# Performance work log

Hardware: AMD Instinct MI355X
Metric: run time of the kernel (lower is better)

Reference implementation:

```python
import jax, jax.numpy as jnp
import numpy as np
from jax import lax

H = 16          # heads
K1, K2 = 3, 3   # kernel_size
LN_EPS = 1e-5


def _ln(x, g, b):
    m = jnp.mean(x, axis=-1, keepdims=True)
    v = jnp.mean(jnp.square(x - m), axis=-1, keepdims=True)
    return (x - m) * lax.rsqrt(v + LN_EPS) * g + b


def _gelu(x):
    return jax.nn.gelu(x, approximate=False)  # torch nn.GELU default (erf)


def setup_inputs() -> dict:
    key = jax.random.key(0)
    B, T, D, Th = 4, 1024, 1024, 256
    C = 2 * D  # context_dim
    ks = jax.random.split(key, 16)

    def w(k, shape):
        fan_in = shape[0]
        return (jax.random.normal(k, shape, jnp.float32) / np.sqrt(fan_in)).astype(jnp.float32)

    inp = {
        'x': jax.random.normal(ks[0], (B, T, D), jnp.float32),
        'historical_data': jax.random.normal(ks[1], (B, Th, D), jnp.float32),
        'Wq': w(ks[2], (D, D)),
        'Wk': w(ks[3], (D, D)),
        'Wv': w(ks[4], (D, D)),
        'hist_W': w(ks[5], (D, C)), 'hist_b': jnp.zeros((C,), jnp.float32),
        'hist_ln_g': jnp.ones((C,), jnp.float32), 'hist_ln_b': jnp.zeros((C,), jnp.float32),
        'ctx_W1': w(ks[6], (C, C // 4)), 'ctx_b1': jnp.zeros((C // 4,), jnp.float32),
        'ctx_W2': w(ks[7], (C // 4, 1)), 'ctx_b2': jnp.zeros((1,), jnp.float32),
        'kg_W1': w(ks[8], (C, D)), 'kg_b1': jnp.zeros((D,), jnp.float32),
        'kg_ln_g': jnp.ones((D,), jnp.float32), 'kg_ln_b': jnp.zeros((D,), jnp.float32),
        'kg_W2': w(ks[9], (D, H * K1 * K2)), 'kg_b2': jnp.zeros((H * K1 * K2,), jnp.float32),
        'proj_W': w(ks[10], (D, D)), 'proj_b': jnp.zeros((D,), jnp.float32),
        'causal_mask': jnp.triu(jnp.ones((T, T), bool), k=1),  # True = masked
    }
    return inp


def reference(x, historical_data, Wq, Wk, Wv, hist_W, hist_b, hist_ln_g, hist_ln_b,
              ctx_W1, ctx_b1, ctx_W2, ctx_b2, kg_W1, kg_b1, kg_ln_g, kg_ln_b,
              kg_W2, kg_b2, proj_W, proj_b, causal_mask):
    B, T, D = x.shape
    hd = D // H
    scale = hd ** -0.5

    # qkv projections (no bias), split heads -> [B, H, T, hd]
    q = (x @ Wq).reshape(B, T, H, hd).transpose(0, 2, 1, 3)
    k = (x @ Wk).reshape(B, T, H, hd).transpose(0, 2, 1, 3)
    v = (x @ Wv).reshape(B, T, H, hd).transpose(0, 2, 1, 3)

    attn = jnp.einsum('bhqd,bhkd->bhqk', q, k) * scale  # [B,H,T,T]

    # --- causal context from history ---
    eh = _gelu(_ln(historical_data @ hist_W + hist_b, hist_ln_g, hist_ln_b))  # [B,Th,C]
    aw = _gelu(eh @ ctx_W1 + ctx_b1) @ ctx_W2 + ctx_b2                        # [B,Th,1]
    aw = jax.nn.softmax(aw, axis=1)
    cc = jnp.sum(eh * aw, axis=1)                                             # [B,C]

    # --- per-(batch,head) 3x3 kernels ---
    kp = _gelu(_ln(cc @ kg_W1 + kg_b1, kg_ln_g, kg_ln_b)) @ kg_W2 + kg_b2     # [B,H*9]
    kernels = jax.nn.softmax(kp.reshape(B, H, K1 * K2), axis=-1)
    kernels = kernels.reshape(B * H, 1, K1, K2)

    # zero masked scores, then mix neighbors via grouped conv2d (cross-correlation)
    mask = causal_mask[None, None]  # [1,1,T,T]
    attn0 = jnp.where(mask, 0.0, attn).reshape(1, B * H, T, T)
    attn = lax.conv_general_dilated(
        attn0, kernels, window_strides=(1, 1),
        padding=((K1 // 2, K1 // 2), (K2 // 2, K2 // 2)),
        feature_group_count=B * H,
        dimension_numbers=('NCHW', 'OIHW', 'NCHW'),
    ).reshape(B, H, T, T)

    attn = jnp.where(mask, -jnp.inf, attn)
    p = jax.nn.softmax(attn, axis=-1)
    out = jnp.einsum('bhqk,bhkd->bhqd', p, v)           # [B,H,T,hd]
    out = out.transpose(0, 2, 1, 3).reshape(B, T, D)
    return out @ proj_W + proj_b
```

## Files before the change

kernel.cpp:

```cpp
#include <hip/hip_runtime.h>
#include <hip/hip_bf16.h>
#include <math.h>

#define DEV static __device__ __forceinline__

typedef __attribute__((ext_vector_type(4))) float f32x4;
typedef __attribute__((ext_vector_type(8))) __bf16 bf16x8;
typedef __attribute__((ext_vector_type(8))) short s16x8;
typedef __attribute__((ext_vector_type(2))) _Float16 h16x2;

DEV float b2f(short v){ unsigned u = ((unsigned)(unsigned short)v) << 16; float f; __builtin_memcpy(&f, &u, 4); return f; }
DEV short f2b(float f){ unsigned u; __builtin_memcpy(&u, &f, 4); unsigned r = (u + 0x7fffu + ((u >> 16) & 1u)) >> 16; return (short)r; }
DEV short f2h(float f){ _Float16 h = (_Float16)f; short s; __builtin_memcpy(&s, &h, 2); return s; }
DEV h16x2 u2h2(unsigned u){ h16x2 h; __builtin_memcpy(&h, &u, 4); return h; }
DEV float gelu_f(float v){ return 0.5f * v * (1.0f + erff(v * 0.70710678118654752f)); }

DEV void gload16(const void* g, void* l) {
  __builtin_amdgcn_global_load_lds((const __attribute__((address_space(1))) unsigned int*)g,
                                   (__attribute__((address_space(3))) unsigned int*)l, 16, 0, 0);
}

DEV void xy_swz(int& bx, int& by, int nx, int ny) {
  int lin = by * nx + bx;
  int q = (nx * ny) >> 3;
  int l2 = (lin & 7) * q + (lin >> 3);
  bx = l2 % nx; by = l2 / nx;
}

__global__ __launch_bounds__(256) void k_cast_all(const float* __restrict__ x, const float* __restrict__ hist,
                                                  short* __restrict__ xb, short* __restrict__ histb){
  int bid = blockIdx.x;
  const float* in; short* out; int i;
  if (bid < 2048) { in = x; out = xb; i = (bid * 256 + threadIdx.x) * 8; }
  else            { in = hist; out = histb; i = ((bid - 2048) * 256 + threadIdx.x) * 8; }
  f32x4 a = *(const f32x4*)&in[i];
  f32x4 b = *(const f32x4*)&in[i + 4];
  s16x8 o;
  o[0]=f2b(a[0]); o[1]=f2b(a[1]); o[2]=f2b(a[2]); o[3]=f2b(a[3]);
  o[4]=f2b(b[0]); o[5]=f2b(b[1]); o[6]=f2b(b[2]); o[7]=f2b(b[3]);
  *(s16x8*)&out[i] = o;
}

__global__ __launch_bounds__(256) void k_zero_qk_pads(short* __restrict__ q, short* __restrict__ kk){
  int idx = blockIdx.x * 256 + threadIdx.x;
  int bh = idx >> 5, c = idx & 31;
  int which = c >> 3, chunk = c & 7;
  short* base = (which < 2) ? q : kk;
  size_t off = (size_t)bh * 1026 * 64 + ((which & 1) ? (size_t)1025 * 64 : 0) + chunk * 8;
  s16x8 zz = {};
  *(s16x8*)&base[off] = zz;
}

DEV void tcast_tile(const float* __restrict__ W, short* __restrict__ Wt, int K, int N, int tx, int ty){
  __shared__ float tile[32][33];
  int nb = tx * 32, kb = ty * 32;
  int tid = threadIdx.x;
  int c = tid & 31, r0 = tid >> 5;
  #pragma unroll
  for (int r = r0; r < 32; r += 8) tile[r][c] = W[(size_t)(kb + r) * N + nb + c];
  __syncthreads();
  #pragma unroll
  for (int r = r0; r < 32; r += 8) Wt[(size_t)(nb + r) * K + kb + c] = f2b(tile[c][r]);
}
__global__ __launch_bounds__(256) void k_tcast_all(const float* __restrict__ Wq, const float* __restrict__ Wk,
                                                   const float* __restrict__ Wv, const float* __restrict__ projW,
                                                   const float* __restrict__ histW, const float* __restrict__ ctxW1,
                                                   short* __restrict__ wqkvt, short* __restrict__ wptb,
                                                   short* __restrict__ whtb, short* __restrict__ wc1tb){
  int bid = blockIdx.x;
  const float* W; short* Wt; int K, N, tx, ty;
  if (bid < 4096) {
    int seg = bid >> 10, t = bid & 1023;
    tx = t & 31; ty = t >> 5; K = 1024; N = 1024;
    if      (seg == 0) { W = Wq;    Wt = wqkvt; }
    else if (seg == 1) { W = Wk;    Wt = wqkvt + 1024*1024; }
    else if (seg == 2) { W = Wv;    Wt = wqkvt + 2*1024*1024; }
    else               { W = projW; Wt = wptb; }
  } else if (bid < 6144) {
    int t = bid - 4096; tx = t & 63; ty = t >> 6; K = 1024; N = 2048; W = histW; Wt = whtb;
  } else {
    int t = bid - 6144; tx = t & 15; ty = t >> 4; K = 2048; N = 512; W = ctxW1; Wt = wc1tb;
  }
  tcast_tile(W, Wt, K, N, tx, ty);
}

DEV void gemm_core(const short* __restrict__ A, const short* __restrict__ Bt,
                   int K, int lda, int ldb, int m0, int n0,
                   short* lA, short* lB, f32x4 acc[4][4])
{
  const int tid = threadIdx.x;
  const int lane = tid & 63;
  const int w = tid >> 6;
  const int wr = (w >> 1) * 64, wc = (w & 1) * 64;
  const int lr = lane & 15, lk = (lane >> 4) * 8;
  for (int kt = 0; kt < K; kt += 64) {
    __syncthreads();
    #pragma unroll
    for (int i = 0; i < 4; ++i) {
      int off = i * 2048 + tid * 8;
      int r = off >> 6, c = off & 63;
      gload16(&A[(size_t)(m0 + r) * lda + kt + c], &lA[off]);
      gload16(&Bt[(size_t)(n0 + r) * ldb + kt + c], &lB[off]);
    }
    __syncthreads();
    #pragma unroll
    for (int kk = 0; kk < 64; kk += 32) {
      bf16x8 af[4], bfr[4];
      #pragma unroll
      for (int mi = 0; mi < 4; ++mi) af[mi] = *(bf16x8*)&lA[(wr + mi*16 + lr)*64 + kk + lk];
      #pragma unroll
      for (int ni = 0; ni < 4; ++ni) bfr[ni] = *(bf16x8*)&lB[(wc + ni*16 + lr)*64 + kk + lk];
      #pragma unroll
      for (int mi = 0; mi < 4; ++mi)
        #pragma unroll
        for (int ni = 0; ni < 4; ++ni)
          acc[mi][ni] = __builtin_amdgcn_mfma_f32_16x16x32_bf16(af[mi], bfr[ni], acc[mi][ni], 0, 0, 0);
    }
  }
}

__global__ __launch_bounds__(256) void k_gemm_f32out(const short* __restrict__ A, const short* __restrict__ Bt,
                                                     float* __restrict__ Cout, const float* __restrict__ bias,
                                                     int N, int K, int doGelu)
{
  __shared__ __align__(16) short lds[2 * 128 * 64];
  f32x4 acc[4][4] = {};
  int bx = blockIdx.x, by = blockIdx.y;
  xy_swz(bx, by, gridDim.x, gridDim.y);
  int m0 = by * 128, n0 = bx * 128;
  gemm_core(A, Bt, K, K, K, m0, n0, lds, lds + 128*64, acc);
  int lane = threadIdx.x & 63, w = threadIdx.x >> 6;
  int wr = (w>>1)*64, wc = (w&1)*64, lr4 = (lane>>4)*4, lc = lane & 15;
  #pragma unroll
  for (int mi = 0; mi < 4; ++mi)
    #pragma unroll
    for (int ni = 0; ni < 4; ++ni)
      #pragma unroll
      for (int r = 0; r < 4; ++r) {
        int row = m0 + wr + mi*16 + lr4 + r;
        int col = n0 + wc + ni*16 + lc;
        float v = acc[mi][ni][r] + bias[col];
        if (doGelu) v = gelu_f(v);
        Cout[(size_t)row * N + col] = v;
      }
}

__global__ __launch_bounds__(256) void k_gemm_qkv(const short* __restrict__ xb, const short* __restrict__ wqkvt,
                                                  short* __restrict__ q, short* __restrict__ kk, short* __restrict__ vt)
{
  __shared__ __align__(16) short lds[128 * 136];
  f32x4 acc[4][4] = {};
  int bx = blockIdx.x, by = blockIdx.y;
  xy_swz(bx, by, gridDim.x, gridDim.y);
  int m0 = by * 128, n0 = bx * 128;
  gemm_core(xb, wqkvt, 1024, 1024, 1024, m0, n0, lds, lds + 128*64, acc);
  int tid = threadIdx.x, lane = tid & 63, w = tid >> 6;
  int wr = (w>>1)*64, wc = (w&1)*64, lr4 = (lane>>4)*4, lc = lane & 15;
  int bb = m0 >> 10, tm0 = m0 & 1023;
  int s = n0 >> 10, dn0 = n0 & 1023;
  __syncthreads();
  if (s < 2) {
    short* dst = (s == 0) ? q : kk;
    #pragma unroll
    for (int mi = 0; mi < 4; ++mi)
      #pragma unroll
      for (int ni = 0; ni < 4; ++ni)
        #pragma unroll
        for (int r = 0; r < 4; ++r)
          lds[(wr + mi*16 + lr4 + r) * 136 + wc + ni*16 + lc] = f2b(acc[mi][ni][r]);
    __syncthreads();
    #pragma unroll
    for (int it = 0; it < 8; ++it) {
      int idx = it * 256 + tid;
      int row = idx >> 4, ch = (idx & 15) * 8;
      int dfull = dn0 + ch;
      *(s16x8*)&dst[((size_t)(bb*16 + (dfull >> 6)) * 1026 + 1 + tm0 + row) * 64 + (dfull & 63)]
          = *(s16x8*)&lds[row * 136 + ch];
    }
  } else {
    #pragma unroll
    for (int mi = 0; mi < 4; ++mi)
      #pragma unroll
      for (int ni = 0; ni < 4; ++ni)
        #pragma unroll
        for (int r = 0; r < 4; ++r)
          lds[(wc + ni*16 + lc) * 136 + wr + mi*16 + lr4 + r] = f2b(acc[mi][ni][r]);
    __syncthreads();
    #pragma unroll
    for (int it = 0; it < 8; ++it) {
      int idx = it * 256 + tid;
      int nl = idx >> 4, mc = (idx & 15) * 8;
      int dfull = dn0 + nl;
      *(s16x8*)&vt[(((size_t)(bb*16 + (dfull >> 6)) * 64 + (dfull & 63)) << 10) + tm0 + mc]
          = *(s16x8*)&lds[nl * 136 + mc];
    }
  }
}

constexpr int ASTR = 152;

DEV void conv_chunk(const short* sS, int g, int c,
                    const h16x2 wp01[3], const h16x2 wp2z[3], float o[8]) {
  #pragma unroll
  for (int dr = 0; dr < 3; ++dr) {
    int base = (g + dr) * ASTR + 8 + c;
    const unsigned* W = (const unsigned*)&sS[base];
    unsigned U0 = W[0], U1 = W[1], U2 = W[2], U3 = W[3];
    unsigned hm1 = (unsigned short)sS[base - 1];
    unsigned hp8 = (unsigned short)sS[base + 8];
    unsigned P0 = hm1 | (U0 << 16);
    unsigned P2 = (U0 >> 16) | (U1 << 16);
    unsigned P4 = (U1 >> 16) | (U2 << 16);
    unsigned P6 = (U2 >> 16) | (U3 << 16);
    unsigned P8 = (U3 >> 16) | (hp8 << 16);
    unsigned P9 = hp8;
    unsigned pr[10] = {P0, U0, P2, U1, P4, U2, P6, U3, P8, P9};
    h16x2 a = wp01[dr], bz = wp2z[dr];
    #pragma unroll
    for (int t = 0; t < 8; ++t) {
      o[t] = __builtin_amdgcn_fdot2(a,  u2h2(pr[t]),     o[t], false);
      o[t] = __builtin_amdgcn_fdot2(bz, u2h2(pr[t + 2]), o[t], false);
    }
  }
}

__global__ __launch_bounds__(512, 4) void k_attn(const short* __restrict__ q, const short* __restrict__ kkg,
                                                 const short* __restrict__ vt, const float* __restrict__ kern,
                                                 short* __restrict__ O)
{
  __shared__ __align__(16) short lQ[130 * 64];
  __shared__ __align__(16) short lK[144 * 64];
  __shared__ __align__(16) short lS[130 * ASTR];
  __shared__ float sInv[128];

  int bh = blockIdx.y, b = bh >> 4, h = bh & 15;
  int qt = (bh >= 32) ? 7 - blockIdx.x : blockIdx.x;
  int m0 = qt * 128;
  int tid = threadIdx.x;
  int w = tid >> 6, lane = tid & 63;
  int lr = lane & 15, lk = (lane >> 4) * 8;

  const short* qp = q   + (size_t)bh * 1026 * 64;
  const short* kp = kkg + (size_t)bh * 1026 * 64;

  h16x2 wp01[3], wp2z[3];
  #pragma unroll
  for (int a = 0; a < 3; ++a) {
    wp01[a][0] = (_Float16)kern[bh * 9 + a * 3 + 0];
    wp01[a][1] = (_Float16)kern[bh * 9 + a * 3 + 1];
    wp2z[a][0] = (_Float16)kern[bh * 9 + a * 3 + 2];
    wp2z[a][1] = (_Float16)0.0f;
  }

  s16x8 zz = {};
  for (int t = tid; t < 130 * 8; t += 512)
    gload16(&qp[((size_t)(m0 + (t >> 3))) * 64 + (t & 7) * 8], &lQ[t * 8]);

  f32x4 pacc[4] = {};
  float psum = 0.0f;
  int g = tid >> 2, qc = tid & 3;

  for (int ct = 0; ct <= qt; ++ct) {
    int n0 = ct * 128;
    for (int t = tid; t < 130 * 8; t += 512)
      gload16(&kp[((size_t)(n0 + (t >> 3))) * 64 + (t & 7) * 8], &lK[t * 8]);
    for (int t = tid; t < 14 * 8; t += 512)
      *(s16x8*)&lK[(130 * 8 + t) * 8] = zz;
    __syncthreads();

    int ntmax = (ct == qt) ? (w + 2) : 9;
    for (int nt = 0; nt < ntmax; ++nt) {
      f32x4 acc = {};
      #pragma unroll
      for (int kk = 0; kk < 64; kk += 32) {
        bf16x8 aq = *(bf16x8*)&lQ[(1 + w * 16 + lr) * 64 + kk + lk];
        bf16x8 bk = *(bf16x8*)&lK[(nt * 16 + lr) * 64 + kk + lk];
        acc = __builtin_amdgcn_mfma_f32_16x16x32_bf16(aq, bk, acc, 0, 0, 0);
      }
      int cloc = nt * 16 + lr - 1;
      if (cloc <= 128) {
        #pragma unroll
        for (int r = 0; r < 4; ++r) {
          int rl = w * 16 + (lane >> 4) * 4 + r;
          float v = acc[r] * 0.125f;
          if (n0 + cloc > m0 + rl) v = 0.0f;
          lS[(rl + 1) * ASTR + 8 + cloc] = f2h(v);
        }
      }
    }
    {
      int hr = -1, hl = 0;
      if (tid < 130) { hr = 0; hl = tid; }
      else if (tid >= 256 && tid < 386) { hr = 129; hl = tid - 256; }
      if (hr >= 0) {
        int cloc = hl - 1;
        int gq = m0 - 1 + hr;
        int gk = n0 + cloc;
        float s = 0.0f;
        if (gq >= 0 && gq < 1024 && gk >= 0 && gk <= gq) {
          #pragma unroll
          for (int kk2 = 0; kk2 < 64; kk2 += 8) {
            s16x8 qv = *(s16x8*)&lQ[hr * 64 + kk2];
            s16x8 kv = *(s16x8*)&lK[(cloc + 1) * 64 + kk2];
            #pragma unroll
            for (int j = 0; j < 8; ++j) s += b2f(qv[j]) * b2f(kv[j]);
          }
          s *= 0.125f;
        }
        lS[hr * ASTR + 8 + cloc] = f2h(s);
      }
    }
    __syncthreads();

    s16x8 ps[4];
    #pragma unroll
    for (int j = 0; j < 4; ++j) {
      int c = qc * 32 + j * 8;
      bool live = (ct < qt) || (c <= g);
      float o[8] = {};
      if (live) conv_chunk(lS, g, c, wp01, wp2z, o);
      int glim = (ct == qt) ? g : 127;
      s16x8 po;
      #pragma unroll
      for (int t = 0; t < 8; ++t) {
        float e = (live && (c + t <= glim)) ? __expf(o[t]) : 0.0f;
        psum += e;
        po[t] = f2b(e);
      }
      ps[j] = po;
    }
    __syncthreads();

    #pragma unroll
    for (int j = 0; j < 4; ++j)
      *(s16x8*)&lS[g * ASTR + 8 + qc * 32 + j * 8] = ps[j];
    __syncthreads();

    int kl = 128;
    if (ct == qt) { kl = ((w * 16 + 16 + 31) >> 5) << 5; if (kl > 128) kl = 128; }
    for (int k0 = 0; k0 < kl; k0 += 32) {
      bf16x8 a = *(bf16x8*)&lS[(w * 16 + lr) * ASTR + 8 + k0 + lk];
      #pragma unroll
      for (int dt = 0; dt < 4; ++dt) {
        bf16x8 bv = *(const bf16x8*)&vt[(((size_t)bh * 64 + dt * 16 + lr) << 10) + n0 + k0 + lk];
        pacc[dt] = __builtin_amdgcn_mfma_f32_16x16x32_bf16(a, bv, pacc[dt], 0, 0, 0);
      }
    }
  }

  psum += __shfl_xor(psum, 1);
  psum += __shfl_xor(psum, 2);
  if (qc == 0) sInv[g] = 1.0f / psum;
  __syncthreads();
  #pragma unroll
  for (int dt = 0; dt < 4; ++dt)
    #pragma unroll
    for (int r = 0; r < 4; ++r) {
      int row = w * 16 + (lane >> 4) * 4 + r;
      float ov = pacc[dt][r] * sInv[row];
      O[((size_t)(b * 1024 + m0 + row) << 10) + h * 64 + dt * 16 + lr] = f2b(ov);
    }
}

__global__ __launch_bounds__(256) void k_ln_gelu2048(const float* __restrict__ x, const float* __restrict__ g,
                                                     const float* __restrict__ be, short* __restrict__ out)
{
  __shared__ float red[8];
  int row = blockIdx.x, tid = threadIdx.x;
  const float* xr = x + (size_t)row * 2048;
  int c0 = tid * 8;
  f32x4 a = *(const f32x4*)&xr[c0];
  f32x4 bb = *(const f32x4*)&xr[c0 + 4];
  float s = 0, s2 = 0;
  #pragma unroll
  for (int t = 0; t < 4; ++t) { s += a[t] + bb[t]; s2 += a[t]*a[t] + bb[t]*bb[t]; }
  #pragma unroll
  for (int off = 32; off; off >>= 1) { s += __shfl_xor(s, off); s2 += __shfl_xor(s2, off); }
  if ((tid & 63) == 0) { red[tid >> 6] = s; red[4 + (tid >> 6)] = s2; }
  __syncthreads();
  s  = red[0] + red[1] + red[2] + red[3];
  s2 = red[4] + red[5] + red[6] + red[7];
  float mean = s * (1.0f / 2048.0f);
  float var  = s2 * (1.0f / 2048.0f) - mean * mean;
  float inv  = rsqrtf(var + 1e-5f);
  f32x4 g0 = *(const f32x4*)&g[c0],  g1 = *(const f32x4*)&g[c0 + 4];
  f32x4 e0 = *(const f32x4*)&be[c0], e1 = *(const f32x4*)&be[c0 + 4];
  s16x8 o;
  #pragma unroll
  for (int t = 0; t < 4; ++t) {
    o[t]     = f2b(gelu_f((a[t]  - mean) * inv * g0[t] + e0[t]));
    o[t + 4] = f2b(gelu_f((bb[t] - mean) * inv * g1[t] + e1[t]));
  }
  *(s16x8*)&out[(size_t)row * 2048 + c0] = o;
}

__global__ __launch_bounds__(256) void k_aw_logit(const float* __restrict__ t, const float* __restrict__ w2,
                                                  const float* __restrict__ b2, float* __restrict__ logit)
{
  int row = blockIdx.x * 4 + (threadIdx.x >> 6);
  int lane = threadIdx.x & 63;
  float s = 0;
  for (int c = lane; c < 512; c += 64) s += t[(size_t)row * 512 + c] * w2[c];
  #pragma unroll
  for (int off = 32; off; off >>= 1) s += __shfl_xor(s, off);
  if (lane == 0) logit[row] = s + b2[0];
}

__global__ __launch_bounds__(256) void k_softmax_cc(const float* __restrict__ logit, const short* __restrict__ ehb,
                                                    float* __restrict__ cc)
{
  __shared__ float sw[256];
  __shared__ float red[8];
  int b = blockIdx.y, ch = blockIdx.x, tid = threadIdx.x;
  float v = logit[b * 256 + tid];
  float m = v;
  #pragma unroll
  for (int off = 32; off; off >>= 1) m = fmaxf(m, __shfl_xor(m, off));
  if ((tid & 63) == 0) red[tid >> 6] = m;
  __syncthreads();
  float M = fmaxf(fmaxf(red[0], red[1]), fmaxf(red[2], red[3]));
  float e = __expf(v - M);
  float s = e;
  #pragma unroll
  for (int off = 32; off; off >>= 1) s += __shfl_xor(s, off);
  if ((tid & 63) == 0) red[4 + (tid >> 6)] = s;
  __syncthreads();
  float invS = 1.0f / (red[4] + red[5] + red[6] + red[7]);
  sw[tid] = e * invS;
  __syncthreads();
  int c = ch * 256 + tid;
  float a = 0;
  for (int t = 0; t < 256; ++t) a += sw[t] * b2f(ehb[(((size_t)(b * 256 + t)) << 11) + c]);
  cc[(b << 11) + c] = a;
}

__global__ __launch_bounds__(256) void k_kg1p(const float* __restrict__ cc, const float* __restrict__ W1,
                                              float* __restrict__ part)
{
  int d = blockIdx.x * 256 + threadIdx.x;
  int kc = blockIdx.y;
  float s0 = 0, s1 = 0, s2 = 0, s3 = 0;
  for (int k = kc * 64; k < kc * 64 + 64; ++k) {
    float w = W1[(size_t)k * 1024 + d];
    s0 += cc[k] * w; s1 += cc[2048 + k] * w; s2 += cc[4096 + k] * w; s3 += cc[6144 + k] * w;
  }
  part[(size_t)(kc * 4 + 0) * 1024 + d] = s0;
  part[(size_t)(kc * 4 + 1) * 1024 + d] = s1;
  part[(size_t)(kc * 4 + 2) * 1024 + d] = s2;
  part[(size_t)(kc * 4 + 3) * 1024 + d] = s3;
}

__global__ __launch_bounds__(256) void k_kg_mid(const float* __restrict__ part, const float* __restrict__ b1,
                                                const float* __restrict__ g, const float* __restrict__ be,
                                                short* __restrict__ kgh)
{
  __shared__ float red[8];
  int b = blockIdx.x, tid = threadIdx.x;
  float v[4]; float s = 0, s2 = 0;
  #pragma unroll
  for (int qi = 0; qi < 4; ++qi) {
    int d = tid + qi * 256;
    float acc = b1[d];
    for (int kc = 0; kc < 32; ++kc) acc += part[(size_t)(kc * 4 + b) * 1024 + d];
    v[qi] = acc; s += acc; s2 += acc * acc;
  }
  #pragma unroll
  for (int off = 32; off; off >>= 1) { s += __shfl_xor(s, off); s2 += __shfl_xor(s2, off); }
  if ((tid & 63) == 0) { red[tid >> 6] = s; red[4 + (tid >> 6)] = s2; }
  __syncthreads();
  s  = red[0] + red[1] + red[2] + red[3];
  s2 = red[4] + red[5] + red[6] + red[7];
  float mean = s * (1.0f / 1024.0f);
  float var  = s2 * (1.0f / 1024.0f) - mean * mean;
  float inv  = rsqrtf(var + 1e-5f);
  #pragma unroll
  for (int qi = 0; qi < 4; ++qi) {
    int d = tid + qi * 256;
    kgh[b * 1024 + d] = f2b(gelu_f((v[qi] - mean) * inv * g[d] + be[d]));
  }
}

__global__ __launch_bounds__(64) void k_kp2(const short* __restrict__ kgh, const float* __restrict__ W2,
                                            const float* __restrict__ b2, float* __restrict__ kern)
{
  int h = blockIdx.x, b = blockIdx.y, lane = threadIdx.x;
  float kg[16];
  #pragma unroll
  for (int m = 0; m < 16; ++m) kg[m] = b2f(kgh[b * 1024 + lane + m * 64]);
  float dj[9];
  #pragma unroll
  for (int j = 0; j < 9; ++j) {
    float s = 0;
    #pragma unroll
    for (int m = 0; m < 16; ++m) s += kg[m] * W2[(size_t)(lane + m * 64) * 144 + h * 9 + j];
    #pragma unroll
    for (int off = 32; off; off >>= 1) s += __shfl_xor(s, off);
    dj[j] = s + b2[h * 9 + j];
  }
  if (lane == 0) {
    float m = dj[0];
    #pragma unroll
    for (int j = 1; j < 9; ++j) m = fmaxf(m, dj[j]);
    float e[9], s = 0;
    #pragma unroll
    for (int j = 0; j < 9; ++j) { e[j] = __expf(dj[j] - m); s += e[j]; }
    float inv = 1.0f / s;
    #pragma unroll
    for (int j = 0; j < 9; ++j) kern[(b * 16 + h) * 9 + j] = e[j] * inv;
  }
}

__global__ void k_fail(float* out){ out[threadIdx.x] = 1.0e9f; }

extern "C" void kernel_launch(void* const* d_in, const int* in_sizes, int n_in,
                              void* d_out, int out_size, void* d_ws, size_t ws_size,
                              hipStream_t stream) {
  (void)in_sizes; (void)n_in; (void)out_size;
  const float* x       = (const float*)d_in[0];
  const float* hist    = (const float*)d_in[1];
  const float* Wq      = (const float*)d_in[2];
  const float* Wk      = (const float*)d_in[3];
  const float* Wv      = (const float*)d_in[4];
  const float* hist_W  = (const float*)d_in[5];
  const float* hist_b  = (const float*)d_in[6];
  const float* hln_g   = (const float*)d_in[7];
  const float* hln_b   = (const float*)d_in[8];
  const float* ctx_W1  = (const float*)d_in[9];
  const float* ctx_b1  = (const float*)d_in[10];
  const float* ctx_W2  = (const float*)d_in[11];
  const float* ctx_b2  = (const float*)d_in[12];
  const float* kg_W1   = (const float*)d_in[13];
  const float* kg_b1   = (const float*)d_in[14];
  const float* kln_g   = (const float*)d_in[15];
  const float* kln_b   = (const float*)d_in[16];
  const float* kg_W2   = (const float*)d_in[17];
  const float* kg_b2   = (const float*)d_in[18];
  const float* proj_W  = (const float*)d_in[19];
  const float* proj_b  = (const float*)d_in[20];
  float* outp = (float*)d_out;

  char* wsb = (char*)d_ws;
  size_t off = 0;
  auto nxt = [&](size_t bytes) { void* p = wsb + off; off += (bytes + 255) & ~(size_t)255; return p; };

  short* xb     = (short*)nxt((size_t)4096*1024*2);
  short* wqkvt  = (short*)nxt((size_t)3*1024*1024*2);
  short* qb     = (short*)nxt((size_t)64*1026*64*2);
  short* kb     = (short*)nxt((size_t)64*1026*64*2);
  short* vtb    = (short*)nxt((size_t)64*64*1024*2);
  short* Ob     = (short*)nxt((size_t)4096*1024*2);
  short* histb  = (short*)nxt((size_t)1024*1024*2);
  short* whtb   = (short*)nxt((size_t)2048*1024*2);
  float* ehpre  = (float*)nxt((size_t)1024*2048*4);
  short* ehb    = (short*)nxt((size_t)1024*2048*2);
  short* wc1tb  = (short*)nxt((size_t)512*2048*2);
  float* tbuf   = (float*)nxt((size_t)1024*512*4);
  float* logit  = (float*)nxt((size_t)1024*4);
  float* ccb    = (float*)nxt((size_t)4*2048*4);
  float* kgpart = (float*)nxt((size_t)128*1024*4);
  short* kghb   = (short*)nxt((size_t)4*1024*2);
  float* kernb  = (float*)nxt((size_t)64*9*4);
  short* wptb   = (short*)nxt((size_t)1024*1024*2);

  if (ws_size < off) { k_fail<<<1, 64, 0, stream>>>(outp); return; }

  k_cast_all<<<2560, 256, 0, stream>>>(x, hist, xb, histb);
  k_zero_qk_pads<<<8, 256, 0, stream>>>(qb, kb);
  k_tcast_all<<<7168, 256, 0, stream>>>(Wq, Wk, Wv, proj_W, hist_W, ctx_W1, wqkvt, wptb, whtb, wc1tb);

  k_gemm_f32out<<<dim3(16, 8), 256, 0, stream>>>(histb, whtb, ehpre, hist_b, 2048, 1024, 0);
  k_ln_gelu2048<<<1024, 256, 0, stream>>>(ehpre, hln_g, hln_b, ehb);
  k_gemm_f32out<<<dim3(4, 8), 256, 0, stream>>>(ehb, wc1tb, tbuf, ctx_b1, 512, 2048, 1);
  k_aw_logit<<<256, 256, 0, stream>>>(tbuf, ctx_W2, ctx_b2, logit);
  k_softmax_cc<<<dim3(8, 4), 256, 0, stream>>>(logit, ehb, ccb);
  k_kg1p<<<dim3(4, 32), 256, 0, stream>>>(ccb, kg_W1, kgpart);
  k_kg_mid<<<4, 256, 0, stream>>>(kgpart, kg_b1, kln_g, kln_b, kghb);
  k_kp2<<<dim3(16, 4), 64, 0, stream>>>(kghb, kg_W2, kg_b2, kernb);

  k_gemm_qkv<<<dim3(24, 32), 256, 0, stream>>>(xb, wqkvt, qb, kb, vtb);
  k_attn<<<dim3(8, 64), 512, 0, stream>>>(qb, kb, vtb, kernb, Ob);
  k_gemm_f32out<<<dim3(8, 32), 256, 0, stream>>>(Ob, wptb, outp, proj_b, 1024, 1024, 0);
}
```

Measured before the change: 310.5 us.

## Split-K small GEMMs, double-buffer K tiles in attention, swizzle LDS, merge pad zeroing

Several independent changes. The hist and ctx GEMMs use split-K across blockIdx.z so more blocks run at once, with bias and GELU moved into the LN kernel and a new reduction kernel. The pad-zeroing kernel is folded into the cast kernel. The attention kernel keeps Q fragments in registers, double-buffers K tiles with an XOR swizzle to prefetch the next tile during compute, and changes the LDS stride and the conv chunk mapping to cut bank conflicts. This adds partial-sum buffers and extra memory traffic for the split-K reduction.

```diff
diff --git a/kernel.cpp b/kernel.cpp
--- a/kernel.cpp
+++ b/kernel.cpp
@@ -28,8 +28,19 @@
 }
 
 __global__ __launch_bounds__(256) void k_cast_all(const float* __restrict__ x, const float* __restrict__ hist,
-                                                  short* __restrict__ xb, short* __restrict__ histb){
+                                                  short* __restrict__ xb, short* __restrict__ histb,
+                                                  short* __restrict__ q, short* __restrict__ kk){
   int bid = blockIdx.x;
+  if (bid >= 2560) {
+    int idx = (bid - 2560) * 256 + threadIdx.x;
+    int bh = idx >> 5, c = idx & 31;
+    int which = c >> 3, chunk = c & 7;
+    short* base = (which < 2) ? q : kk;
+    size_t off = (size_t)bh * 1026 * 64 + ((which & 1) ? (size_t)1025 * 64 : 0) + chunk * 8;
+    s16x8 zz = {};
+    *(s16x8*)&base[off] = zz;
+    return;
+  }
   const float* in; short* out; int i;
   if (bid < 2048) { in = x; out = xb; i = (bid * 256 + threadIdx.x) * 8; }
   else            { in = hist; out = histb; i = ((bid - 2048) * 256 + threadIdx.x) * 8; }
@@ -39,16 +50,6 @@
   o[0]=f2b(a[0]); o[1]=f2b(a[1]); o[2]=f2b(a[2]); o[3]=f2b(a[3]);
   o[4]=f2b(b[0]); o[5]=f2b(b[1]); o[6]=f2b(b[2]); o[7]=f2b(b[3]);
   *(s16x8*)&out[i] = o;
-}
-
-__global__ __launch_bounds__(256) void k_zero_qk_pads(short* __restrict__ q, short* __restrict__ kk){
-  int idx = blockIdx.x * 256 + threadIdx.x;
-  int bh = idx >> 5, c = idx & 31;
-  int which = c >> 3, chunk = c & 7;
-  short* base = (which < 2) ? q : kk;
-  size_t off = (size_t)bh * 1026 * 64 + ((which & 1) ? (size_t)1025 * 64 : 0) + chunk * 8;
-  s16x8 zz = {};
-  *(s16x8*)&base[off] = zz;
 }
 
 DEV void tcast_tile(const float* __restrict__ W, short* __restrict__ Wt, int K, int N, int tx, int ty){
@@ -85,7 +86,7 @@
 }
 
 DEV void gemm_core(const short* __restrict__ A, const short* __restrict__ Bt,
-                   int K, int lda, int ldb, int m0, int n0,
+                   int Ks, int lda, int ldb, int m0, int n0,
                    short* lA, short* lB, f32x4 acc[4][4])
 {
   const int tid = threadIdx.x;
@@ -93,7 +94,7 @@
   const int w = tid >> 6;
   const int wr = (w >> 1) * 64, wc = (w & 1) * 64;
   const int lr = lane & 15, lk = (lane >> 4) * 8;
-  for (int kt = 0; kt < K; kt += 64) {
+  for (int kt = 0; kt < Ks; kt += 64) {
     __syncthreads();
     #pragma unroll
     for (int i = 0; i < 4; ++i) {
@@ -121,14 +122,16 @@
 
 __global__ __launch_bounds__(256) void k_gemm_f32out(const short* __restrict__ A, const short* __restrict__ Bt,
                                                      float* __restrict__ Cout, const float* __restrict__ bias,
-                                                     int N, int K, int doGelu)
+                                                     int N, int lda, int Ks, int mode)
 {
   __shared__ __align__(16) short lds[2 * 128 * 64];
   f32x4 acc[4][4] = {};
   int bx = blockIdx.x, by = blockIdx.y;
   xy_swz(bx, by, gridDim.x, gridDim.y);
   int m0 = by * 128, n0 = bx * 128;
-  gemm_core(A, Bt, K, K, K, m0, n0, lds, lds + 128*64, acc);
+  int koff = blockIdx.z * Ks;
+  gemm_core(A + koff, Bt + koff, Ks, lda, lda, m0, n0, lds, lds + 128*64, acc);
+  Cout += (size_t)blockIdx.z * gridDim.y * 128 * N;
   int lane = threadIdx.x & 63, w = threadIdx.x >> 6;
   int wr = (w>>1)*64, wc = (w&1)*64, lr4 = (lane>>4)*4, lc = lane & 15;
   #pragma unroll
@@ -139,8 +142,9 @@
       for (int r = 0; r < 4; ++r) {
         int row = m0 + wr + mi*16 + lr4 + r;
         int col = n0 + wc + ni*16 + lc;
-        float v = acc[mi][ni][r] + bias[col];
-        if (doGelu) v = gelu_f(v);
+        float v = acc[mi][ni][r];
+        if (mode != 2) v += bias[col];
+        if (mode == 1) v = gelu_f(v);
         Cout[(size_t)row * N + col] = v;
       }
 }
@@ -197,7 +201,7 @@
   }
 }
 
-constexpr int ASTR = 152;
+constexpr int ASTR = 144;
 
 DEV void conv_chunk(const short* sS, int g, int c,
                     const h16x2 wp01[3], const h16x2 wp2z[3], float o[8]) {
@@ -228,8 +232,7 @@
                                                  const short* __restrict__ vt, const float* __restrict__ kern,
                                                  short* __restrict__ O)
 {
-  __shared__ __align__(16) short lQ[130 * 64];
-  __shared__ __align__(16) short lK[144 * 64];
+  __shared__ __align__(16) short lK[2][144 * 64];
   __shared__ __align__(16) short lS[130 * ASTR];
   __shared__ float sInv[128];
 
@@ -252,31 +255,53 @@
     wp2z[a][1] = (_Float16)0.0f;
   }
 
+  bf16x8 qf0, qf1;
+  {
+    const short* qrow = &qp[(size_t)(m0 + 1 + w * 16 + lr) * 64];
+    qf0 = *(const bf16x8*)&qrow[lk];
+    qf1 = *(const bf16x8*)&qrow[32 + lk];
+  }
+  int hr = -1, hl = 0;
+  if (tid < 130) { hr = 0; hl = tid; }
+  else if (tid >= 256 && tid < 386) { hr = 129; hl = tid - 256; }
+
   s16x8 zz = {};
-  for (int t = tid; t < 130 * 8; t += 512)
-    gload16(&qp[((size_t)(m0 + (t >> 3))) * 64 + (t & 7) * 8], &lQ[t * 8]);
+  for (int t = tid; t < 14 * 8; t += 512) {
+    *(s16x8*)&lK[0][(130 * 8 + t) * 8] = zz;
+    *(s16x8*)&lK[1][(130 * 8 + t) * 8] = zz;
+  }
+  for (int t = tid; t < 130 * 8; t += 512) {
+    int r = t >> 3;
+    gload16(&kp[((size_t)r) * 64 + (((t & 7) ^ (r & 7)) << 3)], &lK[0][t * 8]);
+  }
 
   f32x4 pacc[4] = {};
   float psum = 0.0f;
   int g = tid >> 2, qc = tid & 3;
+  int cur = 0;
 
   for (int ct = 0; ct <= qt; ++ct) {
     int n0 = ct * 128;
-    for (int t = tid; t < 130 * 8; t += 512)
-      gload16(&kp[((size_t)(n0 + (t >> 3))) * 64 + (t & 7) * 8], &lK[t * 8]);
-    for (int t = tid; t < 14 * 8; t += 512)
-      *(s16x8*)&lK[(130 * 8 + t) * 8] = zz;
-    __syncthreads();
+    __syncthreads();
+    if (ct < qt) {
+      int n1 = n0 + 128;
+      for (int t = tid; t < 130 * 8; t += 512) {
+        int r = t >> 3;
+        gload16(&kp[((size_t)(n1 + r)) * 64 + (((t & 7) ^ (r & 7)) << 3)], &lK[cur ^ 1][t * 8]);
+      }
+    }
+    const short* lKc = lK[cur];
 
     int ntmax = (ct == qt) ? (w + 2) : 9;
+    int G0 = lk >> 3;
     for (int nt = 0; nt < ntmax; ++nt) {
+      int krow = nt * 16 + lr;
+      int sw = (krow & 7) << 3;
+      bf16x8 bk0 = *(bf16x8*)&lKc[krow * 64 + (( G0      << 3) ^ sw)];
+      bf16x8 bk1 = *(bf16x8*)&lKc[krow * 64 + (((G0 + 4) << 3) ^ sw)];
       f32x4 acc = {};
-      #pragma unroll
-      for (int kk = 0; kk < 64; kk += 32) {
-        bf16x8 aq = *(bf16x8*)&lQ[(1 + w * 16 + lr) * 64 + kk + lk];
-        bf16x8 bk = *(bf16x8*)&lK[(nt * 16 + lr) * 64 + kk + lk];
-        acc = __builtin_amdgcn_mfma_f32_16x16x32_bf16(aq, bk, acc, 0, 0, 0);
-      }
+      acc = __builtin_amdgcn_mfma_f32_16x16x32_bf16(qf0, bk0, acc, 0, 0, 0);
+      acc = __builtin_amdgcn_mfma_f32_16x16x32_bf16(qf1, bk1, acc, 0, 0, 0);
       int cloc = nt * 16 + lr - 1;
       if (cloc <= 128) {
         #pragma unroll
@@ -288,34 +313,30 @@
         }
       }
     }
-    {
-      int hr = -1, hl = 0;
-      if (tid < 130) { hr = 0; hl = tid; }
-      else if (tid >= 256 && tid < 386) { hr = 129; hl = tid - 256; }
-      if (hr >= 0) {
-        int cloc = hl - 1;
-        int gq = m0 - 1 + hr;
-        int gk = n0 + cloc;
-        float s = 0.0f;
-        if (gq >= 0 && gq < 1024 && gk >= 0 && gk <= gq) {
+    if (hr >= 0) {
+      int cloc = hl - 1;
+      float s = 0.0f;
+      if (n0 + cloc <= m0 - 1 + hr) {
+        const short* qrow = &qp[(size_t)(m0 + hr) * 64];
+        int krow = cloc + 1;
+        int swh = (krow & 7) << 3;
+        #pragma unroll
+        for (int G = 0; G < 8; ++G) {
+          s16x8 qv = *(const s16x8*)&qrow[G * 8];
+          s16x8 kv = *(const s16x8*)&lKc[krow * 64 + ((G << 3) ^ swh)];
           #pragma unroll
-          for (int kk2 = 0; kk2 < 64; kk2 += 8) {
-            s16x8 qv = *(s16x8*)&lQ[hr * 64 + kk2];
-            s16x8 kv = *(s16x8*)&lK[(cloc + 1) * 64 + kk2];
-            #pragma unroll
-            for (int j = 0; j < 8; ++j) s += b2f(qv[j]) * b2f(kv[j]);
-          }
-          s *= 0.125f;
+          for (int j = 0; j < 8; ++j) s += b2f(qv[j]) * b2f(kv[j]);
         }
-        lS[hr * ASTR + 8 + cloc] = f2h(s);
+        s *= 0.125f;
       }
+      lS[hr * ASTR + 8 + cloc] = f2h(s);
     }
     __syncthreads();
 
     s16x8 ps[4];
     #pragma unroll
     for (int j = 0; j < 4; ++j) {
-      int c = qc * 32 + j * 8;
+      int c = qc * 8 + j * 32;
       bool live = (ct < qt) || (c <= g);
       float o[8] = {};
       if (live) conv_chunk(lS, g, c, wp01, wp2z, o);
@@ -333,7 +354,7 @@
 
     #pragma unroll
     for (int j = 0; j < 4; ++j)
-      *(s16x8*)&lS[g * ASTR + 8 + qc * 32 + j * 8] = ps[j];
+      *(s16x8*)&lS[g * ASTR + 8 + qc * 8 + j * 32] = ps[j];
     __syncthreads();
 
     int kl = 128;
@@ -346,6 +367,7 @@
         pacc[dt] = __builtin_amdgcn_mfma_f32_16x16x32_bf16(a, bv, pacc[dt], 0, 0, 0);
       }
     }
+    cur ^= 1;
   }
 
   psum += __shfl_xor(psum, 1);
@@ -362,15 +384,21 @@
     }
 }
 
-__global__ __launch_bounds__(256) void k_ln_gelu2048(const float* __restrict__ x, const float* __restrict__ g,
-                                                     const float* __restrict__ be, short* __restrict__ out)
+__global__ __launch_bounds__(256) void k_ln_gelu2048(const float* __restrict__ x, const float* __restrict__ cb,
+                                                     const float* __restrict__ g, const float* __restrict__ be,
+                                                     short* __restrict__ out)
 {
   __shared__ float red[8];
   int row = blockIdx.x, tid = threadIdx.x;
-  const float* xr = x + (size_t)row * 2048;
+  const float* xr0 = x + (size_t)row * 2048;
+  const float* xr1 = x + (size_t)(1024 + row) * 2048;
   int c0 = tid * 8;
-  f32x4 a = *(const f32x4*)&xr[c0];
-  f32x4 bb = *(const f32x4*)&xr[c0 + 4];
+  f32x4 a  = *(const f32x4*)&xr0[c0];
+  f32x4 bb = *(const f32x4*)&xr0[c0 + 4];
+  f32x4 a1 = *(const f32x4*)&xr1[c0];
+  f32x4 b1 = *(const f32x4*)&xr1[c0 + 4];
+  f32x4 cb0 = *(const f32x4*)&cb[c0], cb1 = *(const f32x4*)&cb[c0 + 4];
+  a += a1 + cb0; bb += b1 + cb1;
   float s = 0, s2 = 0;
   #pragma unroll
   for (int t = 0; t < 4; ++t) { s += a[t] + bb[t]; s2 += a[t]*a[t] + bb[t]*bb[t]; }
@@ -392,6 +420,20 @@
     o[t + 4] = f2b(gelu_f((bb[t] - mean) * inv * g1[t] + e1[t]));
   }
   *(s16x8*)&out[(size_t)row * 2048 + c0] = o;
+}
+
+__global__ __launch_bounds__(256) void k_red_gelu(const float* __restrict__ p, const float* __restrict__ b1,
+                                                  float* __restrict__ out)
+{
+  int i = (blockIdx.x * 256 + threadIdx.x) * 4;
+  f32x4 s = *(const f32x4*)&p[i];
+  #pragma unroll
+  for (int z = 1; z < 4; ++z) s += *(const f32x4*)&p[(size_t)z * 524288 + i];
+  f32x4 bv = *(const f32x4*)&b1[i & 511];
+  f32x4 o;
+  #pragma unroll
+  for (int t = 0; t < 4; ++t) o[t] = gelu_f(s[t] + bv[t]);
+  *(f32x4*)&out[i] = o;
 }
 
 __global__ __launch_bounds__(256) void k_aw_logit(const float* __restrict__ t, const float* __restrict__ w2,
@@ -551,9 +593,10 @@
   short* Ob     = (short*)nxt((size_t)4096*1024*2);
   short* histb  = (short*)nxt((size_t)1024*1024*2);
   short* whtb   = (short*)nxt((size_t)2048*1024*2);
-  float* ehpre  = (float*)nxt((size_t)1024*2048*4);
+  float* ehpreP = (float*)nxt((size_t)2*1024*2048*4);
   short* ehb    = (short*)nxt((size_t)1024*2048*2);
   short* wc1tb  = (short*)nxt((size_t)512*2048*2);
+  float* ctxP   = (float*)nxt((size_t)4*1024*512*4);
   float* tbuf   = (float*)nxt((size_t)1024*512*4);
   float* logit  = (float*)nxt((size_t)1024*4);
   float* ccb    = (float*)nxt((size_t)4*2048*4);
@@ -564,13 +607,13 @@
 
   if (ws_size < off) { k_fail<<<1, 64, 0, stream>>>(outp); return; }
 
-  k_cast_all<<<2560, 256, 0, stream>>>(x, hist, xb, histb);
-  k_zero_qk_pads<<<8, 256, 0, stream>>>(qb, kb);
+  k_cast_all<<<2568, 256, 0, stream>>>(x, hist, xb, histb, qb, kb);
   k_tcast_all<<<7168, 256, 0, stream>>>(Wq, Wk, Wv, proj_W, hist_W, ctx_W1, wqkvt, wptb, whtb, wc1tb);
 
-  k_gemm_f32out<<<dim3(16, 8), 256, 0, stream>>>(histb, whtb, ehpre, hist_b, 2048, 1024, 0);
-  k_ln_gelu2048<<<1024, 256, 0, stream>>>(ehpre, hln_g, hln_b, ehb);
-  k_gemm_f32out<<<dim3(4, 8), 256, 0, stream>>>(ehb, wc1tb, tbuf, ctx_b1, 512, 2048, 1);
+  k_gemm_f32out<<<dim3(16, 8, 2), 256, 0, stream>>>(histb, whtb, ehpreP, nullptr, 2048, 1024, 512, 2);
+  k_ln_gelu2048<<<1024, 256, 0, stream>>>(ehpreP, hist_b, hln_g, hln_b, ehb);
+  k_gemm_f32out<<<dim3(4, 8, 4), 256, 0, stream>>>(ehb, wc1tb, ctxP, nullptr, 512, 2048, 512, 2);
+  k_red_gelu<<<512, 256, 0, stream>>>(ctxP, ctx_b1, tbuf);
   k_aw_logit<<<256, 256, 0, stream>>>(tbuf, ctx_W2, ctx_b2, logit);
   k_softmax_cc<<<dim3(8, 4), 256, 0, stream>>>(logit, ehb, ccb);
   k_kg1p<<<dim3(4, 32), 256, 0, stream>>>(ccb, kg_W1, kgpart);
@@ -579,5 +622,5 @@
 
   k_gemm_qkv<<<dim3(24, 32), 256, 0, stream>>>(xb, wqkvt, qb, kb, vtb);
   k_attn<<<dim3(8, 64), 512, 0, stream>>>(qb, kb, vtb, kernb, Ob);
-  k_gemm_f32out<<<dim3(8, 32), 256, 0, stream>>>(Ob, wptb, outp, proj_b, 1024, 1024, 0);
-}
+  k_gemm_f32out<<<dim3(8, 32, 1), 256, 0, stream>>>(Ob, wptb, outp, proj_b, 1024, 1024, 1024, 0);
+}
```

After: 280.9 us. 9.5% less time.
